# Kernel tuning notes

Measured on AMD Instinct MI355X. Metric: run time of the kernel, lower is better.

The kernel has to match this reference:

```python
import jax, jax.numpy as jnp
import numpy as np

D, S, L, W, H, V = 64, 64, 64, 300, 300, 50000
NEG = jnp.float32(-9999999.0)


def setup_inputs() -> dict:
    key = jax.random.key(0)
    ks = jax.random.split(key, 16)
    n = lambda k, shape, s=0.05: jax.random.normal(k, shape, dtype=jnp.float32) * s
    return {
        "word_indices": jax.random.randint(ks[0], (D, S, L), 0, V),
        "E": n(ks[1], (V, W), 0.1),
        "W_sent": n(ks[2], (H, W)), "b_sent": jnp.zeros((H,), jnp.float32),
        "W_par": n(ks[3], (H, H)), "b_par": jnp.zeros((H,), jnp.float32),
        "W_ch": n(ks[4], (H, H)), "b_ch": jnp.zeros((H,), jnp.float32),
        "w_root": n(ks[5], (H,)), "b_root": jnp.zeros((), jnp.float32),
        "root_embed": n(ks[6], (H,)),
        "W_r": n(ks[7], (H, 3 * H)), "b_r": jnp.zeros((H,), jnp.float32),
        "W_cls": n(ks[8], (2, H)), "b_cls": jnp.zeros((2,), jnp.float32),
    }


def reference(word_indices, E, W_sent, b_sent, W_par, b_par, W_ch, b_ch,
              w_root, b_root, root_embed, W_r, b_r, W_cls, b_cls):
    lrelu = lambda x: jax.nn.leaky_relu(x, 0.01)
    # Ragged pad+gather stage of the original, dense here (all lengths == L)
    word_embed = E[word_indices]                 # [D,S,L,W]
    # 0.5*(X[l-1] + reverse(reverse(X))[l-1]) == X[l-1]; LSTM outputs unused in source
    x_last = word_embed[:, :, -1, :]             # [D,S,W]
    enc = lrelu(x_last @ W_sent.T + b_sent)      # [D,S,H] sentence encodings
    # Pairwise parent-child edge scores (O(S^2) dots in the original loops)
    P = lrelu(enc @ W_par.T + b_par)             # [D,S,H]
    C = lrelu(enc @ W_ch.T + b_ch)               # [D,S,H]
    A = jnp.einsum('dih,djh->dij', P, C)         # [D,S,S]
    A = jnp.where(jnp.eye(S, dtype=bool)[None], NEG, A)
    A = jax.nn.softmax(A, axis=1)                # Softmax(dim=0) per doc: over parents i
    scores = enc @ w_root + b_root               # [D,S] root scores
    fri = jax.nn.softmax(scores, axis=1)         # Softmax(dim=0) over sentences
    # ri[i] = r_embeds([enc_i, sum_k A[k,i]*enc_k + fri_i*root, enc_i*sum_k A[i,k]])
    tmp = jnp.einsum('dki,dkh->dih', A, enc)     # [D,S,H]
    agg = tmp + fri[..., None] * root_embed      # [D,S,H]
    tmp3 = enc * A.sum(axis=2, keepdims=True)    # [D,S,H]
    ri = lrelu(jnp.concatenate([enc, agg, tmp3], axis=-1) @ W_r.T + b_r)  # [D,S,H]
    final = ri.mean(axis=1)                      # [D,H]
    out = final @ W_cls.T + b_cls                # [D,2]
    return out, A, fri
```

## Files before the change

kernel.cpp:

```cpp
#include <hip/hip_runtime.h>
#include <hip/hip_bf16.h>

#define NEG_INF (-9999999.0f)

typedef __attribute__((ext_vector_type(8))) short bf16x8;
typedef __attribute__((ext_vector_type(4))) float f32x4;
typedef unsigned short us;

__device__ __forceinline__ float b2f(us u) {
  union { unsigned int i; float f; } x; x.i = ((unsigned int)u) << 16; return x.f;
}
__device__ __forceinline__ us f2b(float f) {
  union { float f; unsigned int i; } x; x.f = f;
  unsigned int r = x.i + 0x7fffu + ((x.i >> 16) & 1u);
  return (us)(r >> 16);
}
__device__ __forceinline__ float lrelu(float v) { return v > 0.f ? v : 0.01f * v; }
__device__ __forceinline__ bf16x8 ld8(const us* p) { return *reinterpret_cast<const bf16x8*>(p); }

__global__ __launch_bounds__(256) void k_prep(const int* __restrict__ wi, const float* __restrict__ E,
    const float* __restrict__ Ws, const float* __restrict__ Wp, const float* __restrict__ Wc,
    const float* __restrict__ Wr,
    us* __restrict__ Wsb, us* __restrict__ Wpb, us* __restrict__ Wcb, us* __restrict__ Wrb,
    us* __restrict__ xg, us* __restrict__ encb, us* __restrict__ Pb, us* __restrict__ Cb,
    us* __restrict__ encTb) {
  int task = blockIdx.y;
  int gid = blockIdx.x * 256 + threadIdx.x;
  const int stride = 640 * 256;
  if (task < 3) {
    const float* src = (task == 0) ? Ws : (task == 1) ? Wp : Wc;
    us* dst = (task == 0) ? Wsb : (task == 1) ? Wpb : Wcb;
    for (int i = gid; i < 304 * 320; i += stride) {
      int r = i / 320, c = i - r * 320;
      dst[i] = (r < 300 && c < 300) ? f2b(src[r * 300 + c]) : 0;
    }
  } else if (task == 3) {
    for (int i = gid; i < 304 * 928; i += stride) {
      int r = i / 928, c = i - r * 928;
      Wrb[i] = (r < 300 && c < 900) ? f2b(Wr[r * 900 + c]) : 0;
    }
  } else if (task == 4) {
    for (int i = gid; i < 4096 * 320; i += stride) {
      int r = i / 320, c = i - r * 320;
      xg[i] = (c < 300) ? f2b(E[(long)wi[r * 64 + 63] * 300 + c]) : 0;
    }
  } else if (task == 5) {
    for (int i = gid; i < 3 * 4096 * 20; i += stride) {
      int b = i / 81920, rem = i - b * 81920;
      int r = rem / 20, c = 300 + (rem - r * 20);
      us* dst = (b == 0) ? encb : (b == 1) ? Pb : Cb;
      dst[r * 320 + c] = 0;
    }
  } else {
    for (int i = gid; i < 4 * 4096; i += stride)
      encTb[300 * 4096 + i] = 0;
  }
}

__device__ __forceinline__ void stage16(const us* __restrict__ g, us* lds, int units, int t) {
  const float4* s = reinterpret_cast<const float4*>(g);
  float4* d = reinterpret_cast<float4*>(lds);
  for (int i = t; i < units; i += 256) d[i] = s[i];
}

template<int NT, int KP>
__device__ __forceinline__ void sweep_lds(const us* As, const us* __restrict__ Bb,
    int bpitch, int nt0, int lo, int q, int ksn, f32x4* acc) {
  const us* ar = As + lo * KP + 8 * q;
  const us* br[NT];
#pragma unroll
  for (int t = 0; t < NT; ++t)
    br[t] = Bb + (long)((nt0 + t) * 16 + lo) * bpitch + 8 * q;
  bf16x8 b0[NT], b1[NT], b2[NT];
#pragma unroll
  for (int t = 0; t < NT; ++t) b0[t] = ld8(br[t]);
#pragma unroll
  for (int t = 0; t < NT; ++t) b1[t] = ld8(br[t] + 32);
#pragma unroll
  for (int t = 0; t < NT; ++t) b2[t] = ld8(br[t] + 64);
  bf16x8 a0 = *reinterpret_cast<const bf16x8*>(ar);
  for (int ks = 0; ks < ksn - 3; ++ks) {
    bf16x8 a1 = *reinterpret_cast<const bf16x8*>(ar + (ks + 1) * 32);
    bf16x8 bn[NT];
#pragma unroll
    for (int t = 0; t < NT; ++t) bn[t] = ld8(br[t] + (ks + 3) * 32);
#pragma unroll
    for (int t = 0; t < NT; ++t)
      acc[t] = __builtin_amdgcn_mfma_f32_16x16x32_bf16(a0, b0[t], acc[t], 0, 0, 0);
    a0 = a1;
#pragma unroll
    for (int t = 0; t < NT; ++t) { b0[t] = b1[t]; b1[t] = b2[t]; b2[t] = bn[t]; }
  }
  {
    bf16x8 a1 = *reinterpret_cast<const bf16x8*>(ar + (ksn - 2) * 32);
#pragma unroll
    for (int t = 0; t < NT; ++t)
      acc[t] = __builtin_amdgcn_mfma_f32_16x16x32_bf16(a0, b0[t], acc[t], 0, 0, 0);
    a0 = a1;
#pragma unroll
    for (int t = 0; t < NT; ++t) b0[t] = b1[t];
  }
  {
    bf16x8 a1 = *reinterpret_cast<const bf16x8*>(ar + (ksn - 1) * 32);
#pragma unroll
    for (int t = 0; t < NT; ++t)
      acc[t] = __builtin_amdgcn_mfma_f32_16x16x32_bf16(a0, b0[t], acc[t], 0, 0, 0);
    a0 = a1;
#pragma unroll
    for (int t = 0; t < NT; ++t) b0[t] = b2[t];
  }
#pragma unroll
  for (int t = 0; t < NT; ++t)
    acc[t] = __builtin_amdgcn_mfma_f32_16x16x32_bf16(a0, b0[t], acc[t], 0, 0, 0);
}

template<int NT>
__device__ __forceinline__ void sweep(const us* __restrict__ Ab, int apitch,
    const us* __restrict__ Bb, int bpitch, int m0, int nt0, int lo, int q,
    int ks0, int ksn, f32x4* acc) {
  const us* ar = Ab + (long)(m0 + lo) * apitch + 8 * q + (long)ks0 * 32;
  const us* br[NT];
#pragma unroll
  for (int t = 0; t < NT; ++t)
    br[t] = Bb + (long)((nt0 + t) * 16 + lo) * bpitch + 8 * q + (long)ks0 * 32;
  bf16x8 a0 = ld8(ar), a1 = ld8(ar + 32);
  bf16x8 b0[NT], b1[NT];
#pragma unroll
  for (int t = 0; t < NT; ++t) b0[t] = ld8(br[t]);
#pragma unroll
  for (int t = 0; t < NT; ++t) b1[t] = ld8(br[t] + 32);
  for (int ks = 0; ks < ksn - 2; ++ks) {
    bf16x8 a2 = ld8(ar + (ks + 2) * 32);
    bf16x8 b2[NT];
#pragma unroll
    for (int t = 0; t < NT; ++t) b2[t] = ld8(br[t] + (ks + 2) * 32);
#pragma unroll
    for (int t = 0; t < NT; ++t)
      acc[t] = __builtin_amdgcn_mfma_f32_16x16x32_bf16(a0, b0[t], acc[t], 0, 0, 0);
    a0 = a1; a1 = a2;
#pragma unroll
    for (int t = 0; t < NT; ++t) { b0[t] = b1[t]; b1[t] = b2[t]; }
  }
#pragma unroll
  for (int t = 0; t < NT; ++t)
    acc[t] = __builtin_amdgcn_mfma_f32_16x16x32_bf16(a0, b0[t], acc[t], 0, 0, 0);
#pragma unroll
  for (int t = 0; t < NT; ++t)
    acc[t] = __builtin_amdgcn_mfma_f32_16x16x32_bf16(a1, b1[t], acc[t], 0, 0, 0);
}

template<int NT>
__device__ __forceinline__ void epi_bf16(const f32x4* acc, const float* __restrict__ bias,
    us* __restrict__ outb, us* __restrict__ outT,
    int m0, int nt0, int lo, int q) {
#pragma unroll
  for (int t = 0; t < NT; ++t) {
    int col = (nt0 + t) * 16 + lo;
    if (col >= 300) continue;
    float bb = bias[col];
#pragma unroll
    for (int r = 0; r < 4; ++r) {
      int row = m0 + q * 4 + r;
      us h = f2b(lrelu(acc[t][r] + bb));
      outb[(long)row * 320 + col] = h;
      if (outT) outT[(long)col * 4096 + row] = h;
    }
  }
}

__global__ __launch_bounds__(256) void k_gemm_enc(const us* __restrict__ Ab,
    const us* __restrict__ Bb, const float* __restrict__ bias,
    us* __restrict__ encb, us* __restrict__ encTb) {
  __shared__ __align__(16) us As[16 * 320];
  int t = threadIdx.x;
  int m0 = blockIdx.x * 16;
  stage16(Ab + (long)m0 * 320, As, 640, t);
  __syncthreads();
  int w = t >> 6, lane = t & 63, lo = lane & 15, q = lane >> 4;
  f32x4 z = {0.f, 0.f, 0.f, 0.f};
  if (w < 3) {
    f32x4 acc[5] = {z, z, z, z, z};
    sweep_lds<5, 320>(As, Bb, 320, w * 5, lo, q, 10, acc);
    epi_bf16<5>(acc, bias, encb, encTb, m0, w * 5, lo, q);
  } else {
    f32x4 acc[4] = {z, z, z, z};
    sweep_lds<4, 320>(As, Bb, 320, 15, lo, q, 10, acc);
    epi_bf16<4>(acc, bias, encb, encTb, m0, 15, lo, q);
  }
}

__global__ __launch_bounds__(256) void k_gemm_pc(const us* __restrict__ Ab,
    const us* __restrict__ Wpb, const us* __restrict__ Wcb,
    const float* __restrict__ bp, const float* __restrict__ bc,
    us* __restrict__ Pb, us* __restrict__ Cb) {
  __shared__ __align__(16) us As[16 * 320];
  int which = blockIdx.y;
  const us* Bb = which ? Wcb : Wpb;
  const float* bias = which ? bc : bp;
  us* outb = which ? Cb : Pb;
  int t = threadIdx.x;
  int m0 = blockIdx.x * 16;
  stage16(Ab + (long)m0 * 320, As, 640, t);
  __syncthreads();
  int w = t >> 6, lane = t & 63, lo = lane & 15, q = lane >> 4;
  f32x4 z = {0.f, 0.f, 0.f, 0.f};
  if (w < 3) {
    f32x4 acc[5] = {z, z, z, z, z};
    sweep_lds<5, 320>(As, Bb, 320, w * 5, lo, q, 10, acc);
    epi_bf16<5>(acc, bias, outb, (us*)nullptr, m0, w * 5, lo, q);
  } else {
    f32x4 acc[4] = {z, z, z, z};
    sweep_lds<4, 320>(As, Bb, 320, 15, lo, q, 10, acc);
    epi_bf16<4>(acc, bias, outb, (us*)nullptr, m0, 15, lo, q);
  }
}

__global__ __launch_bounds__(256) void k_attn(
    const us* __restrict__ Pb, const us* __restrict__ Cb, const us* __restrict__ encb,
    const float* __restrict__ w_root, const float* __restrict__ b_root,
    float* __restrict__ Aout, float* __restrict__ outF,
    us* __restrict__ Atb, float* __restrict__ rsp) {
  __shared__ float Ls[64][17];
  __shared__ float pm[4][16], psum[4][16];
  __shared__ float scores[64];
  int d = blockIdx.x, jg = blockIdx.y, t = threadIdx.x;
  int w = t >> 6, lane = t & 63, lo = lane & 15, q = lane >> 4;

  if (jg == 0) {
    int rr = t >> 2, quad = t & 3;
    const us* er = encb + (long)(d * 64 + rr) * 320;
    float s = 0.f;
    for (int h = quad * 4; h + 4 <= 300; h += 16) {
      ushort4 e4 = *reinterpret_cast<const ushort4*>(er + h);
      s = fmaf(b2f(e4.x), w_root[h], s);
      s = fmaf(b2f(e4.y), w_root[h + 1], s);
      s = fmaf(b2f(e4.z), w_root[h + 2], s);
      s = fmaf(b2f(e4.w), w_root[h + 3], s);
    }
    s += __shfl_xor(s, 1);
    s += __shfl_xor(s, 2);
    if (quad == 0) scores[rr] = s + b_root[0];
    __syncthreads();
    if (t < 64) {
      float sc = scores[t];
      float m = sc;
#pragma unroll
      for (int o = 32; o > 0; o >>= 1) m = fmaxf(m, __shfl_xor(m, o, 64));
      float e = expf(sc - m);
      float sum = e;
#pragma unroll
      for (int o = 32; o > 0; o >>= 1) sum += __shfl_xor(sum, o, 64);
      outF[d * 64 + t] = e / sum;
    }
  }

  {
    const us* Pd = Pb + (long)d * 64 * 320;
    const us* Cd = Cb + (long)d * 64 * 320;
    f32x4 acc = {0.f, 0.f, 0.f, 0.f};
    sweep<1>(Pd, 320, Cd, 320, w * 16, jg, lo, q, 0, 10, &acc);
#pragma unroll
    for (int r = 0; r < 4; ++r) {
      int i = w * 16 + q * 4 + r, j = jg * 16 + lo;
      Ls[i][lo] = (i == j) ? NEG_INF : acc[r];
    }
  }
  __syncthreads();

  {
    int col = t & 15, p = t >> 4;
    if (t < 64) {
      float mx = -3.0e38f;
      for (int i = p * 16; i < p * 16 + 16; ++i) mx = fmaxf(mx, Ls[i][col]);
      pm[p][col] = mx;
    }
    __syncthreads();
    if (t < 64) {
      float gmx = fmaxf(fmaxf(pm[0][col], pm[1][col]), fmaxf(pm[2][col], pm[3][col]));
      float s = 0.f;
      for (int i = p * 16; i < p * 16 + 16; ++i) s += expf(Ls[i][col] - gmx);
      psum[p][col] = s;
    }
    __syncthreads();
    if (t < 64) {
      float gmx = fmaxf(fmaxf(pm[0][col], pm[1][col]), fmaxf(pm[2][col], pm[3][col]));
      float inv = 1.f / (psum[0][col] + psum[1][col] + psum[2][col] + psum[3][col]);
      int j = jg * 16 + col;
      float* Ad = Aout + (long)d * 4096;
      us* Atd = Atb + (long)d * 4096;
      for (int i = p * 16; i < p * 16 + 16; ++i) {
        float a = expf(Ls[i][col] - gmx) * inv;
        Ad[i * 64 + j] = a;
        Atd[j * 64 + i] = f2b(a);
        Ls[i][col] = a;
      }
    }
  }
  __syncthreads();
  if (t < 64) {
    float s = 0.f;
#pragma unroll
    for (int c = 0; c < 16; ++c) s += Ls[t][c];
    rsp[(d * 4 + jg) * 64 + t] = s;
  }
}

__global__ __launch_bounds__(256) void k_glue2(
    const us* __restrict__ Atb, const us* __restrict__ encTb, const us* __restrict__ encb,
    const float* __restrict__ outF, const float* __restrict__ rsp,
    const float* __restrict__ root, us* __restrict__ ub) {
  __shared__ float frs[64], rs[64];
  int d = blockIdx.x, g = blockIdx.y, t = threadIdx.x;
  if (t < 64) {
    frs[t] = outF[d * 64 + t];
    rs[t] = rsp[(d * 4 + 0) * 64 + t] + rsp[(d * 4 + 1) * 64 + t]
          + rsp[(d * 4 + 2) * 64 + t] + rsp[(d * 4 + 3) * 64 + t];
  }
  __syncthreads();
  int w = t >> 6, lane = t & 63, lo = lane & 15, q = lane >> 4;
  int ht = g * 4 + w;
  if (ht < 19) {
    const us* Atd = Atb + (long)d * 4096;
    bf16x8 av0[4], av1[4];
#pragma unroll
    for (int mt = 0; mt < 4; ++mt) {
      av0[mt] = ld8(Atd + (mt * 16 + lo) * 64 + 8 * q);
      av1[mt] = ld8(Atd + (mt * 16 + lo) * 64 + 32 + 8 * q);
    }
    const us* brow = encTb + (long)(ht * 16 + lo) * 4096 + d * 64 + 8 * q;
    bf16x8 bv0 = ld8(brow), bv1 = ld8(brow + 32);
    int h = ht * 16 + lo;
    float rt = (h < 300) ? root[h] : 0.f;
#pragma unroll
    for (int mt = 0; mt < 4; ++mt) {
      f32x4 acc = {0.f, 0.f, 0.f, 0.f};
      acc = __builtin_amdgcn_mfma_f32_16x16x32_bf16(av0[mt], bv0, acc, 0, 0, 0);
      acc = __builtin_amdgcn_mfma_f32_16x16x32_bf16(av1[mt], bv1, acc, 0, 0, 0);
      if (h < 300) {
#pragma unroll
        for (int r = 0; r < 4; ++r) {
          int i = mt * 16 + q * 4 + r;
          ub[(long)(d * 64 + i) * 928 + 300 + h] = f2b(acc[r] + frs[i] * rt);
        }
      }
    }
  }
  for (int idx = t; idx < 64 * 60; idx += 256) {
    int r = idx / 60, c = g * 60 + (idx - (idx / 60) * 60);
    us ev = encb[(long)(d * 64 + r) * 320 + c];
    ub[(long)(d * 64 + r) * 928 + c] = ev;
    ub[(long)(d * 64 + r) * 928 + 600 + c] = f2b(b2f(ev) * rs[r]);
  }
  if (g == 4) {
    for (int idx = t; idx < 64 * 28; idx += 256) {
      int r = idx / 28, c = 900 + (idx - r * 28);
      ub[(long)(d * 64 + r) * 928 + c] = 0;
    }
  }
}

__global__ __launch_bounds__(256) void k_gemm_ri(const us* __restrict__ Ab,
    const us* __restrict__ Bb, const float* __restrict__ bias, float* __restrict__ ri) {
  __shared__ __align__(16) us As[16 * 928];
  int t = threadIdx.x;
  int m0 = blockIdx.x * 16;
  stage16(Ab + (long)m0 * 928, As, 1856, t);
  __syncthreads();
  int w = t >> 6, lane = t & 63, lo = lane & 15, q = lane >> 4;
  f32x4 z = {0.f, 0.f, 0.f, 0.f};
  if (w < 3) {
    f32x4 acc[5] = {z, z, z, z, z};
    sweep_lds<5, 928>(As, Bb, 928, w * 5, lo, q, 29, acc);
#pragma unroll
    for (int t2 = 0; t2 < 5; ++t2) {
      int col = (w * 5 + t2) * 16 + lo;
      if (col >= 300) continue;
      float bb = bias[col];
#pragma unroll
      for (int r = 0; r < 4; ++r)
        ri[(long)(m0 + q * 4 + r) * 300 + col] = lrelu(acc[t2][r] + bb);
    }
  } else {
    f32x4 acc[4] = {z, z, z, z};
    sweep_lds<4, 928>(As, Bb, 928, 15, lo, q, 29, acc);
#pragma unroll
    for (int t2 = 0; t2 < 4; ++t2) {
      int col = (15 + t2) * 16 + lo;
      if (col >= 300) continue;
      float bb = bias[col];
#pragma unroll
      for (int r = 0; r < 4; ++r)
        ri[(long)(m0 + q * 4 + r) * 300 + col] = lrelu(acc[t2][r] + bb);
    }
  }
}

__global__ __launch_bounds__(256) void k_final(const float* __restrict__ ri,
    const float* __restrict__ W_cls, const float* __restrict__ b_cls,
    float* __restrict__ outp) {
  __shared__ float fin[300];
  __shared__ float red[256];
  int d = blockIdx.x, t = threadIdx.x;
  for (int h = t; h < 300; h += 256) {
    float s = 0.f;
    for (int i = 0; i < 64; ++i) s += ri[((d * 64) + i) * 300 + h];
    fin[h] = s * (1.0f / 64.0f);
  }
  __syncthreads();
  for (int c2 = 0; c2 < 2; ++c2) {
    float pth = 0.f;
    for (int h = t; h < 300; h += 256) pth = fmaf(fin[h], W_cls[c2 * 300 + h], pth);
    red[t] = pth;
    __syncthreads();
    for (int o = 128; o > 0; o >>= 1) {
      if (t < o) red[t] += red[t + o];
      __syncthreads();
    }
    if (t == 0) outp[d * 2 + c2] = red[0] + b_cls[c2];
    __syncthreads();
  }
}

extern "C" void kernel_launch(void* const* d_in, const int* in_sizes, int n_in,
                              void* d_out, int out_size, void* d_ws, size_t ws_size,
                              hipStream_t stream) {
  const int*   wi     = (const int*)d_in[0];
  const float* E      = (const float*)d_in[1];
  const float* W_sent = (const float*)d_in[2];
  const float* b_sent = (const float*)d_in[3];
  const float* W_par  = (const float*)d_in[4];
  const float* b_par  = (const float*)d_in[5];
  const float* W_ch   = (const float*)d_in[6];
  const float* b_ch   = (const float*)d_in[7];
  const float* w_root = (const float*)d_in[8];
  const float* b_root = (const float*)d_in[9];
  const float* root_e = (const float*)d_in[10];
  const float* W_r    = (const float*)d_in[11];
  const float* b_r    = (const float*)d_in[12];
  const float* W_cls  = (const float*)d_in[13];
  const float* b_cls  = (const float*)d_in[14];

  us* B = (us*)d_ws;
  us* Wsb   = B;
  us* Wpb   = B + 97280;
  us* Wcb   = B + 194560;
  us* Wrb   = B + 291840;
  us* xg    = B + 573952;
  us* encb  = B + 1884672;
  us* encTb = B + 3195392;
  us* Pb    = B + 4440576;
  us* Cb    = B + 5751296;
  us* ub    = B + 7062016;
  us* Atb   = B + 10863104;
  float* rsp = (float*)(B + 11125248);
  float* ri  = (float*)(B + 11157760);

  float* outp = (float*)d_out;
  float* outA = outp + 128;
  float* outF = outp + 128 + 262144;

  k_prep<<<dim3(640, 7), 256, 0, stream>>>(wi, E, W_sent, W_par, W_ch, W_r,
                                           Wsb, Wpb, Wcb, Wrb, xg, encb, Pb, Cb, encTb);
  k_gemm_enc<<<256, 256, 0, stream>>>(xg, Wsb, b_sent, encb, encTb);
  k_gemm_pc<<<dim3(256, 2), 256, 0, stream>>>(encb, Wpb, Wcb, b_par, b_ch, Pb, Cb);
  k_attn<<<dim3(64, 4), 256, 0, stream>>>(Pb, Cb, encb, w_root, b_root,
                                          outA, outF, Atb, rsp);
  k_glue2<<<dim3(64, 5), 256, 0, stream>>>(Atb, encTb, encb, outF, rsp, root_e, ub);
  k_gemm_ri<<<256, 256, 0, stream>>>(ub, Wrb, b_r, ri);
  k_final<<<64, 256, 0, stream>>>(ri, W_cls, b_cls, outp);
}
```

Before: 189.0 us.

## Split W_r by linearity and reorder A-aggregation after projection

Uses linearity to split the concat @ W_r^T product into three separate projections: enc@W1, enc@W2 (stored transposed) and enc@W3. These run in the same launch as the P/C GEMMs. A combine kernel then applies A^T to the W2-projected values, adds the root term precomputed as W2·root and the rowsum scaling of the W3 term, then applies the bias and leaky ReLU. This removes the 928-wide concatenated buffer, its build kernel and the separate ri GEMM, at the cost of fp32 intermediate round trips through memory and a different rounding order.

```diff
diff --git a/kernel.cpp b/kernel.cpp
--- a/kernel.cpp
+++ b/kernel.cpp
@@ -20,10 +20,10 @@
 
 __global__ __launch_bounds__(256) void k_prep(const int* __restrict__ wi, const float* __restrict__ E,
     const float* __restrict__ Ws, const float* __restrict__ Wp, const float* __restrict__ Wc,
-    const float* __restrict__ Wr,
-    us* __restrict__ Wsb, us* __restrict__ Wpb, us* __restrict__ Wcb, us* __restrict__ Wrb,
+    const float* __restrict__ Wr, const float* __restrict__ root,
+    us* __restrict__ Wsb, us* __restrict__ Wpb, us* __restrict__ Wcb, us* __restrict__ Wspl,
     us* __restrict__ xg, us* __restrict__ encb, us* __restrict__ Pb, us* __restrict__ Cb,
-    us* __restrict__ encTb) {
+    us* __restrict__ encTb, us* __restrict__ Y2Tb, float* __restrict__ r2) {
   int task = blockIdx.y;
   int gid = blockIdx.x * 256 + threadIdx.x;
   const int stride = 640 * 256;
@@ -35,9 +35,10 @@
       dst[i] = (r < 300 && c < 300) ? f2b(src[r * 300 + c]) : 0;
     }
   } else if (task == 3) {
-    for (int i = gid; i < 304 * 928; i += stride) {
-      int r = i / 928, c = i - r * 928;
-      Wrb[i] = (r < 300 && c < 900) ? f2b(Wr[r * 900 + c]) : 0;
+    for (int i = gid; i < 3 * 97280; i += stride) {
+      int sub = i / 97280, rem = i - sub * 97280;
+      int r = rem / 320, c = rem - r * 320;
+      Wspl[i] = (r < 300 && c < 300) ? f2b(Wr[r * 900 + sub * 300 + c]) : 0;
     }
   } else if (task == 4) {
     for (int i = gid; i < 4096 * 320; i += stride) {
@@ -51,9 +52,17 @@
       us* dst = (b == 0) ? encb : (b == 1) ? Pb : Cb;
       dst[r * 320 + c] = 0;
     }
+  } else if (task == 6) {
+    for (int i = gid; i < 2 * 4 * 4096; i += stride) {
+      if (i < 16384) encTb[300 * 4096 + i] = 0;
+      else           Y2Tb[300 * 4096 + (i - 16384)] = 0;
+    }
   } else {
-    for (int i = gid; i < 4 * 4096; i += stride)
-      encTb[300 * 4096 + i] = 0;
+    if (gid < 300) {
+      float s = 0.f;
+      for (int w = 0; w < 300; ++w) s = fmaf(Wr[gid * 900 + 300 + w], root[w], s);
+      r2[gid] = s;
+    }
   }
 }
 
@@ -165,6 +174,32 @@
       outb[(long)row * 320 + col] = h;
       if (outT) outT[(long)col * 4096 + row] = h;
     }
+  }
+}
+
+template<int NT>
+__device__ __forceinline__ void epi_f32lin(const f32x4* acc, float* __restrict__ out,
+    int m0, int nt0, int lo, int q) {
+#pragma unroll
+  for (int t = 0; t < NT; ++t) {
+    int col = (nt0 + t) * 16 + lo;
+    if (col >= 300) continue;
+#pragma unroll
+    for (int r = 0; r < 4; ++r)
+      out[(long)(m0 + q * 4 + r) * 300 + col] = acc[t][r];
+  }
+}
+
+template<int NT>
+__device__ __forceinline__ void epi_b16T(const f32x4* acc, us* __restrict__ outT,
+    int m0, int nt0, int lo, int q) {
+#pragma unroll
+  for (int t = 0; t < NT; ++t) {
+    int col = (nt0 + t) * 16 + lo;
+    if (col >= 300) continue;
+#pragma unroll
+    for (int r = 0; r < 4; ++r)
+      outT[(long)col * 4096 + m0 + q * 4 + r] = f2b(acc[t][r]);
   }
 }
 
@@ -189,29 +224,38 @@
   }
 }
 
-__global__ __launch_bounds__(256) void k_gemm_pc(const us* __restrict__ Ab,
+__global__ __launch_bounds__(256) void k_big(const us* __restrict__ encb,
     const us* __restrict__ Wpb, const us* __restrict__ Wcb,
+    const us* __restrict__ W1b, const us* __restrict__ W2b, const us* __restrict__ W3b,
     const float* __restrict__ bp, const float* __restrict__ bc,
-    us* __restrict__ Pb, us* __restrict__ Cb) {
+    us* __restrict__ Pb, us* __restrict__ Cb,
+    float* __restrict__ Y1, us* __restrict__ Y2Tb, float* __restrict__ Y3) {
   __shared__ __align__(16) us As[16 * 320];
-  int which = blockIdx.y;
-  const us* Bb = which ? Wcb : Wpb;
-  const float* bias = which ? bc : bp;
-  us* outb = which ? Cb : Pb;
   int t = threadIdx.x;
   int m0 = blockIdx.x * 16;
-  stage16(Ab + (long)m0 * 320, As, 640, t);
+  int which = blockIdx.y;
+  stage16(encb + (long)m0 * 320, As, 640, t);
   __syncthreads();
   int w = t >> 6, lane = t & 63, lo = lane & 15, q = lane >> 4;
+  const us* Bb = (which == 0) ? Wpb : (which == 1) ? Wcb
+               : (which == 2) ? W2b : (which == 3) ? W1b : W3b;
   f32x4 z = {0.f, 0.f, 0.f, 0.f};
   if (w < 3) {
     f32x4 acc[5] = {z, z, z, z, z};
     sweep_lds<5, 320>(As, Bb, 320, w * 5, lo, q, 10, acc);
-    epi_bf16<5>(acc, bias, outb, (us*)nullptr, m0, w * 5, lo, q);
+    if (which == 0)      epi_bf16<5>(acc, bp, Pb, (us*)nullptr, m0, w * 5, lo, q);
+    else if (which == 1) epi_bf16<5>(acc, bc, Cb, (us*)nullptr, m0, w * 5, lo, q);
+    else if (which == 2) epi_b16T<5>(acc, Y2Tb, m0, w * 5, lo, q);
+    else if (which == 3) epi_f32lin<5>(acc, Y1, m0, w * 5, lo, q);
+    else                 epi_f32lin<5>(acc, Y3, m0, w * 5, lo, q);
   } else {
     f32x4 acc[4] = {z, z, z, z};
     sweep_lds<4, 320>(As, Bb, 320, 15, lo, q, 10, acc);
-    epi_bf16<4>(acc, bias, outb, (us*)nullptr, m0, 15, lo, q);
+    if (which == 0)      epi_bf16<4>(acc, bp, Pb, (us*)nullptr, m0, 15, lo, q);
+    else if (which == 1) epi_bf16<4>(acc, bc, Cb, (us*)nullptr, m0, 15, lo, q);
+    else if (which == 2) epi_b16T<4>(acc, Y2Tb, m0, 15, lo, q);
+    else if (which == 3) epi_f32lin<4>(acc, Y1, m0, 15, lo, q);
+    else                 epi_f32lin<4>(acc, Y3, m0, 15, lo, q);
   }
 }
 
@@ -305,10 +349,12 @@
   }
 }
 
-__global__ __launch_bounds__(256) void k_glue2(
-    const us* __restrict__ Atb, const us* __restrict__ encTb, const us* __restrict__ encb,
+__global__ __launch_bounds__(256) void k_comb(
+    const us* __restrict__ Atb, const us* __restrict__ Y2Tb,
+    const float* __restrict__ Y1, const float* __restrict__ Y3,
     const float* __restrict__ outF, const float* __restrict__ rsp,
-    const float* __restrict__ root, us* __restrict__ ub) {
+    const float* __restrict__ r2, const float* __restrict__ b_r,
+    float* __restrict__ ri) {
   __shared__ float frs[64], rs[64];
   int d = blockIdx.x, g = blockIdx.y, t = threadIdx.x;
   if (t < 64) {
@@ -319,78 +365,32 @@
   __syncthreads();
   int w = t >> 6, lane = t & 63, lo = lane & 15, q = lane >> 4;
   int ht = g * 4 + w;
-  if (ht < 19) {
-    const us* Atd = Atb + (long)d * 4096;
-    bf16x8 av0[4], av1[4];
-#pragma unroll
-    for (int mt = 0; mt < 4; ++mt) {
-      av0[mt] = ld8(Atd + (mt * 16 + lo) * 64 + 8 * q);
-      av1[mt] = ld8(Atd + (mt * 16 + lo) * 64 + 32 + 8 * q);
-    }
-    const us* brow = encTb + (long)(ht * 16 + lo) * 4096 + d * 64 + 8 * q;
-    bf16x8 bv0 = ld8(brow), bv1 = ld8(brow + 32);
-    int h = ht * 16 + lo;
-    float rt = (h < 300) ? root[h] : 0.f;
-#pragma unroll
-    for (int mt = 0; mt < 4; ++mt) {
-      f32x4 acc = {0.f, 0.f, 0.f, 0.f};
-      acc = __builtin_amdgcn_mfma_f32_16x16x32_bf16(av0[mt], bv0, acc, 0, 0, 0);
-      acc = __builtin_amdgcn_mfma_f32_16x16x32_bf16(av1[mt], bv1, acc, 0, 0, 0);
-      if (h < 300) {
-#pragma unroll
-        for (int r = 0; r < 4; ++r) {
-          int i = mt * 16 + q * 4 + r;
-          ub[(long)(d * 64 + i) * 928 + 300 + h] = f2b(acc[r] + frs[i] * rt);
-        }
+  if (ht >= 19) return;
+  const us* Atd = Atb + (long)d * 4096;
+  bf16x8 av0[4], av1[4];
+#pragma unroll
+  for (int mt = 0; mt < 4; ++mt) {
+    av0[mt] = ld8(Atd + (mt * 16 + lo) * 64 + 8 * q);
+    av1[mt] = ld8(Atd + (mt * 16 + lo) * 64 + 32 + 8 * q);
+  }
+  const us* brow = Y2Tb + (long)(ht * 16 + lo) * 4096 + d * 64 + 8 * q;
+  bf16x8 bv0 = ld8(brow), bv1 = ld8(brow + 32);
+  int h = ht * 16 + lo;
+  float bb = (h < 300) ? b_r[h] : 0.f;
+  float rr2 = (h < 300) ? r2[h] : 0.f;
+#pragma unroll
+  for (int mt = 0; mt < 4; ++mt) {
+    f32x4 acc = {0.f, 0.f, 0.f, 0.f};
+    acc = __builtin_amdgcn_mfma_f32_16x16x32_bf16(av0[mt], bv0, acc, 0, 0, 0);
+    acc = __builtin_amdgcn_mfma_f32_16x16x32_bf16(av1[mt], bv1, acc, 0, 0, 0);
+    if (h < 300) {
+#pragma unroll
+      for (int r = 0; r < 4; ++r) {
+        int i = mt * 16 + q * 4 + r;
+        long idx = (long)(d * 64 + i) * 300 + h;
+        float v = Y1[idx] + rs[i] * Y3[idx] + acc[r] + frs[i] * rr2 + bb;
+        ri[idx] = lrelu(v);
       }
-    }
-  }
-  for (int idx = t; idx < 64 * 60; idx += 256) {
-    int r = idx / 60, c = g * 60 + (idx - (idx / 60) * 60);
-    us ev = encb[(long)(d * 64 + r) * 320 + c];
-    ub[(long)(d * 64 + r) * 928 + c] = ev;
-    ub[(long)(d * 64 + r) * 928 + 600 + c] = f2b(b2f(ev) * rs[r]);
-  }
-  if (g == 4) {
-    for (int idx = t; idx < 64 * 28; idx += 256) {
-      int r = idx / 28, c = 900 + (idx - r * 28);
-      ub[(long)(d * 64 + r) * 928 + c] = 0;
-    }
-  }
-}
-
-__global__ __launch_bounds__(256) void k_gemm_ri(const us* __restrict__ Ab,
-    const us* __restrict__ Bb, const float* __restrict__ bias, float* __restrict__ ri) {
-  __shared__ __align__(16) us As[16 * 928];
-  int t = threadIdx.x;
-  int m0 = blockIdx.x * 16;
-  stage16(Ab + (long)m0 * 928, As, 1856, t);
-  __syncthreads();
-  int w = t >> 6, lane = t & 63, lo = lane & 15, q = lane >> 4;
-  f32x4 z = {0.f, 0.f, 0.f, 0.f};
-  if (w < 3) {
-    f32x4 acc[5] = {z, z, z, z, z};
-    sweep_lds<5, 928>(As, Bb, 928, w * 5, lo, q, 29, acc);
-#pragma unroll
-    for (int t2 = 0; t2 < 5; ++t2) {
-      int col = (w * 5 + t2) * 16 + lo;
-      if (col >= 300) continue;
-      float bb = bias[col];
-#pragma unroll
-      for (int r = 0; r < 4; ++r)
-        ri[(long)(m0 + q * 4 + r) * 300 + col] = lrelu(acc[t2][r] + bb);
-    }
-  } else {
-    f32x4 acc[4] = {z, z, z, z};
-    sweep_lds<4, 928>(As, Bb, 928, 15, lo, q, 29, acc);
-#pragma unroll
-    for (int t2 = 0; t2 < 4; ++t2) {
-      int col = (15 + t2) * 16 + lo;
-      if (col >= 300) continue;
-      float bb = bias[col];
-#pragma unroll
-      for (int r = 0; r < 4; ++r)
-        ri[(long)(m0 + q * 4 + r) * 300 + col] = lrelu(acc[t2][r] + bb);
     }
   }
 }
@@ -444,28 +444,35 @@
   us* Wsb   = B;
   us* Wpb   = B + 97280;
   us* Wcb   = B + 194560;
-  us* Wrb   = B + 291840;
-  us* xg    = B + 573952;
-  us* encb  = B + 1884672;
-  us* encTb = B + 3195392;
-  us* Pb    = B + 4440576;
-  us* Cb    = B + 5751296;
-  us* ub    = B + 7062016;
-  us* Atb   = B + 10863104;
-  float* rsp = (float*)(B + 11125248);
-  float* ri  = (float*)(B + 11157760);
+  us* Wspl  = B + 291840;
+  us* W1b   = Wspl;
+  us* W2b   = Wspl + 97280;
+  us* W3b   = Wspl + 194560;
+  us* xg    = B + 583680;
+  us* encb  = B + 1894400;
+  us* encTb = B + 3205120;
+  us* Pb    = B + 4450304;
+  us* Cb    = B + 5761024;
+  us* Y2Tb  = B + 7071744;
+  us* Atb   = B + 8316928;
+  float* rsp = (float*)(B + 8579072);
+  float* r2  = (float*)(B + 8611840);
+  float* Y1  = (float*)(B + 8612440);
+  float* Y3  = (float*)(B + 11070040);
+  float* ri  = (float*)(B + 13527640);
 
   float* outp = (float*)d_out;
   float* outA = outp + 128;
   float* outF = outp + 128 + 262144;
 
-  k_prep<<<dim3(640, 7), 256, 0, stream>>>(wi, E, W_sent, W_par, W_ch, W_r,
-                                           Wsb, Wpb, Wcb, Wrb, xg, encb, Pb, Cb, encTb);
+  k_prep<<<dim3(640, 8), 256, 0, stream>>>(wi, E, W_sent, W_par, W_ch, W_r, root_e,
+                                           Wsb, Wpb, Wcb, Wspl, xg, encb, Pb, Cb,
+                                           encTb, Y2Tb, r2);
   k_gemm_enc<<<256, 256, 0, stream>>>(xg, Wsb, b_sent, encb, encTb);
-  k_gemm_pc<<<dim3(256, 2), 256, 0, stream>>>(encb, Wpb, Wcb, b_par, b_ch, Pb, Cb);
+  k_big<<<dim3(256, 5), 256, 0, stream>>>(encb, Wpb, Wcb, W1b, W2b, W3b,
+                                          b_par, b_ch, Pb, Cb, Y1, Y2Tb, Y3);
   k_attn<<<dim3(64, 4), 256, 0, stream>>>(Pb, Cb, encb, w_root, b_root,
                                           outA, outF, Atb, rsp);
-  k_glue2<<<dim3(64, 5), 256, 0, stream>>>(Atb, encTb, encb, outF, rsp, root_e, ub);
-  k_gemm_ri<<<256, 256, 0, stream>>>(ub, Wrb, b_r, ri);
+  k_comb<<<dim3(64, 5), 256, 0, stream>>>(Atb, Y2Tb, Y1, Y3, outF, rsp, r2, b_r, ri);
   k_final<<<64, 256, 0, stream>>>(ri, W_cls, b_cls, outp);
 }
```

After: 195.6 us. +3.5%, slower.
